# Performance work log

Measured on AMD Instinct MI355X. Metric: run time of the kernel, lower is better.

The kernel has to match this reference:

```python
import jax, jax.numpy as jnp
import numpy as np

COST_CLASS, COST_BBOX, COST_MASK = 1.0, 5.0, 2.0
EPS = 1e-6


def setup_inputs() -> dict:
    key = jax.random.key(0)
    k = jax.random.split(key, 8)
    B, Q, M, C1, H, W = 8, 300, 100, 81, 128, 128
    pred_logits = jax.random.normal(k[0], (B, Q, C1), jnp.float32)
    # boxes as valid xyxy in [0,1]: lo in [0,.5], size in [0,.5]
    plo = jax.random.uniform(k[1], (B, Q, 2)) * 0.5
    psz = jax.random.uniform(k[2], (B, Q, 2)) * 0.5
    pred_boxes = jnp.concatenate([plo, plo + psz], axis=-1)
    pred_masks = jax.random.normal(k[3], (B, Q, H, W), jnp.float32)
    gt_labels = jax.random.randint(k[4], (B, M), 0, C1, dtype=jnp.int32)
    glo = jax.random.uniform(k[5], (B, M, 2)) * 0.5
    gsz = jax.random.uniform(k[6], (B, M, 2)) * 0.5
    gt_boxes = jnp.concatenate([glo, glo + gsz], axis=-1)
    gt_masks = (jax.random.uniform(k[7], (B, M, H, W)) > 0.5).astype(jnp.float32)
    valid = jnp.ones((B, M), jnp.bool_)
    return dict(pred_logits=pred_logits, pred_boxes=pred_boxes, pred_masks=pred_masks,
                gt_labels=gt_labels, gt_boxes=gt_boxes, gt_masks=gt_masks, valid=valid)


def _giou(b1, b2):
    # b1 [Q,4], b2 [M,4] (xyxy) -> [Q,M] generalized IoU
    lt = jnp.maximum(b1[:, None, :2], b2[None, :, :2])
    rb = jnp.minimum(b1[:, None, 2:], b2[None, :, 2:])
    wh = jnp.clip(rb - lt, 0.0)
    inter = wh[..., 0] * wh[..., 1]
    a1 = (b1[:, 2] - b1[:, 0]) * (b1[:, 3] - b1[:, 1])
    a2 = (b2[:, 2] - b2[:, 0]) * (b2[:, 3] - b2[:, 1])
    union = a1[:, None] + a2[None, :] - inter
    iou = inter / (union + EPS)
    ltm = jnp.minimum(b1[:, None, :2], b2[None, :, :2])
    rbm = jnp.maximum(b1[:, None, 2:], b2[None, :, 2:])
    whm = jnp.clip(rbm - ltm, 0.0)
    am = whm[..., 0] * whm[..., 1]
    return iou - (am - union) / (am + EPS)


@jax.jit
def _cost_matrix(pred_logits, pred_boxes, pred_masks, gt_labels, gt_boxes, gt_masks):
    B, Q = pred_logits.shape[:2]
    M = gt_labels.shape[1]
    probs = jax.nn.softmax(pred_logits, axis=-1)                      # [B,Q,C+1]
    idx = jnp.broadcast_to(gt_labels[:, None, :].astype(jnp.int32), (B, Q, M))
    cost_class = -jnp.take_along_axis(probs, idx, axis=2)             # [B,Q,M]
    # L1 cdist
    cost_bbox = jnp.abs(pred_boxes[:, :, None, :] - gt_boxes[:, None, :, :]).sum(-1)
    cost_giou = -jax.vmap(_giou)(pred_boxes, gt_boxes)                # [B,Q,M]
    # dice cost
    pm = jax.nn.sigmoid(pred_masks).reshape(B, Q, -1)                 # [B,Q,HW]
    gm = gt_masks.reshape(B, M, -1).astype(pm.dtype)                  # [B,M,HW]
    num = 2.0 * jnp.einsum('bqc,bmc->bqm', pm, gm)
    den = pm.sum(-1)[:, :, None] + gm.sum(-1)[:, None, :]
    cost_mask = 1.0 - num / (den + EPS)
    # NOTE: faithful to source quirk -- giou term is folded into cost_bbox
    # and therefore weighted by COST_BBOX.
    return (COST_CLASS * cost_class + COST_BBOX * (cost_bbox + cost_giou)
            + COST_MASK * cost_mask)


def _hungarian(cost):
    # Jonker-Volgenant style shortest-augmenting-path assignment (e-maxx).
    # cost: np [n,m] with n <= m. Returns p[m]: row assigned to each col (-1 if none).
    n, m = cost.shape
    u = np.zeros(n)
    v = np.zeros(m)
    p = np.full(m, -1, np.int64)
    for i in range(n):
        minv = np.full(m, np.inf)
        way = np.full(m, -1, np.int64)
        used = np.zeros(m, bool)
        cur_row, j0 = i, -1
        while True:
            cur = cost[cur_row] - u[cur_row] - v
            upd = (~used) & (cur < minv)
            minv[upd] = cur[upd]
            way[upd] = j0
            mv = np.where(used, np.inf, minv)
            j1 = int(np.argmin(mv))
            delta = mv[j1]
            u[i] += delta
            uj = np.nonzero(used)[0]
            if uj.size:
                u[p[uj]] += delta
                v[uj] -= delta
            minv[~used] -= delta
            used[j1] = True
            j0 = j1
            cur_row = p[j1]
            if cur_row == -1:
                break
        j = j0
        while j != -1:
            jp = way[j]
            p[j] = p[jp] if jp != -1 else i
            j = jp
    return p


def reference(pred_logits, pred_boxes, pred_masks, gt_labels, gt_boxes, gt_masks, valid):
    # valid is all-ones (num_gt == max_objects for every sample), so the
    # per-sample variable-size slicing in the torch loop reduces to full M.
    C = _cost_matrix(pred_logits, pred_boxes, pred_masks, gt_labels, gt_boxes, gt_masks)
    Cn = np.asarray(C, dtype=np.float64)
    preds, gts = [], []
    for b in range(Cn.shape[0]):
        # solve on transpose: rows = gt (M=100) <= cols = queries (Q=300)
        p = _hungarian(Cn[b].T)            # p[q] = matched gt index or -1
        q = np.nonzero(p >= 0)[0]          # sorted pred indices (scipy convention)
        preds.append(q)
        gts.append(p[q])
    pred_idx = jnp.asarray(np.stack(preds), dtype=jnp.int32)  # [B, M]
    gt_idx = jnp.asarray(np.stack(gts), dtype=jnp.int32)      # [B, M]
    return C, pred_idx, gt_idx
```

## Files before the change

### kernel.cpp

```cpp
#include <hip/hip_runtime.h>

#define HW 16384
#define NQ 300
#define NM 100
#define NB 8
#define NC 81
#define KCH 4096
#define CTP 304

typedef __attribute__((ext_vector_type(8))) short frag8;
typedef __attribute__((ext_vector_type(4))) float float4v;
typedef __attribute__((ext_vector_type(4))) unsigned short ushort4v;

__device__ __forceinline__ unsigned short f2bf(float f) {
  union { float f; unsigned u; } c; c.f = f;
  unsigned r = c.u + 0x7FFFu + ((c.u >> 16) & 1u);
  return (unsigned short)(r >> 16);
}

__global__ __launch_bounds__(256) void prep_kernel(
    const float* __restrict__ pmask, const float* __restrict__ gmask,
    unsigned short* __restrict__ pm, unsigned short* __restrict__ gm,
    float* __restrict__ psum, float* __restrict__ gsum) {
  int row = blockIdx.x;
  int t = threadIdx.x;
  bool isP = row < NB * NQ;
  const float* srcf = isP ? (pmask + (size_t)row * HW)
                          : (gmask + (size_t)(row - NB * NQ) * HW);
  unsigned short* dst = isP ? (pm + (size_t)row * HW)
                            : (gm + (size_t)(row - NB * NQ) * HW);
  const float4v* src = (const float4v*)srcf;
  float s = 0.f;
  for (int i = t; i < HW / 4; i += 256) {
    float4v x = src[i];
    float y0, y1, y2, y3;
    if (isP) {
      y0 = 1.f / (1.f + __expf(-x.x));
      y1 = 1.f / (1.f + __expf(-x.y));
      y2 = 1.f / (1.f + __expf(-x.z));
      y3 = 1.f / (1.f + __expf(-x.w));
    } else { y0 = x.x; y1 = x.y; y2 = x.z; y3 = x.w; }
    s += (y0 + y1) + (y2 + y3);
    ushort4v o = { f2bf(y0), f2bf(y1), f2bf(y2), f2bf(y3) };
    *(ushort4v*)(dst + i * 4) = o;
  }
  for (int off = 32; off > 0; off >>= 1) s += __shfl_xor(s, off, 64);
  __shared__ float red[4];
  int wave = t >> 6, lane = t & 63;
  if (lane == 0) red[wave] = s;
  __syncthreads();
  if (t == 0) {
    float tot = (red[0] + red[1]) + (red[2] + red[3]);
    if (isP) psum[row] = tot; else gsum[row - NB * NQ] = tot;
  }
}

__global__ __launch_bounds__(256) void softmax_kernel(
    const float* __restrict__ logits, float* __restrict__ probs) {
  int wave = threadIdx.x >> 6, lane = threadIdx.x & 63;
  int row = blockIdx.x * 4 + wave;
  const float* in = logits + (size_t)row * NC;
  float x0 = (lane < NC) ? in[lane] : -1e30f;
  float x1 = (lane + 64 < NC) ? in[lane + 64] : -1e30f;
  float mx = fmaxf(x0, x1);
  for (int off = 32; off > 0; off >>= 1) mx = fmaxf(mx, __shfl_xor(mx, off, 64));
  float e0 = (lane < NC) ? __expf(x0 - mx) : 0.f;
  float e1 = (lane + 64 < NC) ? __expf(x1 - mx) : 0.f;
  float s = e0 + e1;
  for (int off = 32; off > 0; off >>= 1) s += __shfl_xor(s, off, 64);
  float inv = 1.f / s;
  if (lane < NC) probs[(size_t)row * NC + lane] = e0 * inv;
  if (lane + 64 < NC) probs[(size_t)row * NC + lane + 64] = e1 * inv;
}

__global__ __launch_bounds__(64) void dot_kernel(
    const unsigned short* __restrict__ pm, const unsigned short* __restrict__ gm,
    float* __restrict__ part) {
  int qt = blockIdx.x;
  int b = blockIdx.y >> 2, kc = blockIdx.y & 3;
  int lane = threadIdx.x;
  int q0 = qt * 16;
  int row_a = q0 + (lane & 15);
  int ra = (row_a < NQ) ? row_a : NQ - 1;
  int koff = (lane >> 4) * 8;
  const unsigned short* pA = pm + ((size_t)b * NQ + ra) * HW + kc * KCH + koff;
  const unsigned short* pB0 = gm + (size_t)b * NM * HW + kc * KCH + koff;
  const unsigned short* pB[7];
#pragma unroll
  for (int mt = 0; mt < 7; ++mt) {
    int row_b = mt * 16 + (lane & 15);
    int rb = (row_b < NM) ? row_b : NM - 1;
    pB[mt] = pB0 + (size_t)rb * HW;
  }
  float4v acc[7];
#pragma unroll
  for (int mt = 0; mt < 7; ++mt) acc[mt] = (float4v){0.f, 0.f, 0.f, 0.f};
#pragma unroll 2
  for (int k = 0; k < KCH; k += 32) {
    frag8 a = *(const frag8*)(pA + k);
#pragma unroll
    for (int mt = 0; mt < 7; ++mt) {
      frag8 bb = *(const frag8*)(pB[mt] + k);
      acc[mt] = __builtin_amdgcn_mfma_f32_16x16x32_bf16(a, bb, acc[mt], 0, 0, 0);
    }
  }
#pragma unroll
  for (int mt = 0; mt < 7; ++mt) {
    int cm = mt * 16 + (lane & 15);
    if (cm < NM) {
#pragma unroll
      for (int r = 0; r < 4; ++r) {
        int cq = q0 + (lane >> 4) * 4 + r;
        if (cq < NQ)
          part[(size_t)kc * (NB * NQ * NM) + ((size_t)b * NQ + cq) * NM + cm] = acc[mt][r];
      }
    }
  }
}

__global__ __launch_bounds__(256) void combine_kernel(
    const float* __restrict__ part, const float* __restrict__ psum,
    const float* __restrict__ gsum, const float* __restrict__ probs,
    const int* __restrict__ labels, const float* __restrict__ pboxes,
    const float* __restrict__ gboxes, float* __restrict__ outC,
    float* __restrict__ ct) {
  int idx = blockIdx.x * 256 + threadIdx.x;
  if (idx >= NB * NQ * NM) return;
  int b = idx / (NQ * NM);
  int r = idx - b * (NQ * NM);
  int q = r / NM;
  int m = r - q * NM;
  const int STRIDE = NB * NQ * NM;
  float num = 2.f * (part[idx] + part[STRIDE + idx] + part[2 * STRIDE + idx] + part[3 * STRIDE + idx]);
  float den = psum[b * NQ + q] + gsum[b * NM + m];
  float cmask = 1.f - num / (den + 1e-6f);
  int lab = labels[b * NM + m];
  float cclass = -probs[((size_t)b * NQ + q) * NC + lab];
  const float* pb = pboxes + ((size_t)b * NQ + q) * 4;
  const float* gb = gboxes + ((size_t)b * NM + m) * 4;
  float p0 = pb[0], p1 = pb[1], p2 = pb[2], p3 = pb[3];
  float g0 = gb[0], g1 = gb[1], g2 = gb[2], g3 = gb[3];
  float cbbox = fabsf(p0 - g0) + fabsf(p1 - g1) + fabsf(p2 - g2) + fabsf(p3 - g3);
  float iw = fmaxf(fminf(p2, g2) - fmaxf(p0, g0), 0.f);
  float ih = fmaxf(fminf(p3, g3) - fmaxf(p1, g1), 0.f);
  float inter = iw * ih;
  float a1 = (p2 - p0) * (p3 - p1), a2 = (g2 - g0) * (g3 - g1);
  float uni = a1 + a2 - inter;
  float iou = inter / (uni + 1e-6f);
  float aw = fmaxf(fmaxf(p2, g2) - fminf(p0, g0), 0.f);
  float ah = fmaxf(fmaxf(p3, g3) - fminf(p1, g1), 0.f);
  float am = aw * ah;
  float giou = iou - (am - uni) / (am + 1e-6f);
  float C = cclass + 5.f * (cbbox - giou) + 2.f * cmask;
  outC[idx] = C;
  ct[((size_t)b * NM + m) * CTP + q] = C;
}

extern __shared__ char hsmem[];
__global__ __launch_bounds__(64) void hungarian_kernel(
    const float* __restrict__ ct, float* __restrict__ out) {
  float* cost = (float*)hsmem;
  float* u = (float*)(hsmem + 121600);
  int* p = (int*)(hsmem + 122000);
  int* way = (int*)(hsmem + 123280);
  const int b = blockIdx.x;
  const int lane = threadIdx.x;
  const float* a = ct + (size_t)b * NM * CTP;

  for (int i = lane; i < NM * CTP; i += 64) cost[i] = a[i];
  for (int k = lane; k < NM; k += 64) u[k] = 0.f;
  float v[5], minv[5];
  int usedR[5];
#pragma unroll
  for (int w = 0; w < 5; ++w) {
    p[lane + 64 * w] = -1;
    v[w] = 0.f;
  }
  __syncthreads();

  for (int i = 0; i < NM; ++i) {
#pragma unroll
    for (int w = 0; w < 5; ++w) {
      int j = lane + 64 * w;
      minv[w] = __builtin_inff();
      usedR[w] = (j >= NQ) ? 1 : 0;
      way[j] = -1;
    }
    int cur_row = i;
    int j0 = -1;
    __builtin_amdgcn_wave_barrier();
    while (true) {
      float urow = u[cur_row];
      unsigned long long best = ~0ull;
#pragma unroll
      for (int w = 0; w < 5; ++w) {
        if (!usedR[w]) {
          int j = lane + 64 * w;
          float cur = cost[cur_row * CTP + j] - urow - v[w];
          if (cur < minv[w]) { minv[w] = cur; way[j] = j0; }
          unsigned sb = __float_as_uint(minv[w]);
          sb = (sb >> 31) ? ~sb : (sb | 0x80000000u);
          unsigned long long key = ((unsigned long long)sb << 32) | (unsigned)j;
          if (key < best) best = key;
        }
      }
      for (int off = 32; off > 0; off >>= 1) {
        unsigned long long o = __shfl_xor(best, off, 64);
        if (o < best) best = o;
      }
      int j1 = (int)(best & 0xFFFFFFFFu);
      unsigned sb = (unsigned)(best >> 32);
      float delta = __uint_as_float((sb >> 31) ? (sb ^ 0x80000000u) : ~sb);
      __builtin_amdgcn_wave_barrier();
#pragma unroll
      for (int w = 0; w < 5; ++w) {
        int j = lane + 64 * w;
        if (j < NQ) {
          if (usedR[w]) {
            v[w] -= delta;
            int pj = p[j];
            u[pj] += delta;
          } else {
            minv[w] -= delta;
          }
        }
      }
      if (lane == 0) u[i] += delta;
      __builtin_amdgcn_wave_barrier();
#pragma unroll
      for (int w = 0; w < 5; ++w) {
        if (lane + 64 * w == j1) usedR[w] = 1;
      }
      int nr = p[j1];
      j0 = j1;
      if (nr < 0) break;
      cur_row = nr;
    }
    __builtin_amdgcn_wave_barrier();
    if (lane == 0) {
      int j = j0;
      while (j != -1) {
        int jp = way[j];
        p[j] = (jp != -1) ? p[jp] : i;
        j = jp;
      }
    }
    __builtin_amdgcn_wave_barrier();
    __syncthreads();
  }
  if (lane == 0) {
    float* po = out + NB * NQ * NM + b * NM;
    float* go = out + NB * NQ * NM + NB * NM + b * NM;
    int cnt = 0;
    for (int j = 0; j < NQ; ++j) {
      int pj = p[j];
      if (pj >= 0) { po[cnt] = (float)j; go[cnt] = (float)pj; ++cnt; }
    }
  }
}

extern "C" void kernel_launch(void* const* d_in, const int* in_sizes, int n_in,
                              void* d_out, int out_size, void* d_ws, size_t ws_size,
                              hipStream_t stream) {
  const float* logits = (const float*)d_in[0];
  const float* pboxes = (const float*)d_in[1];
  const float* pmask  = (const float*)d_in[2];
  const int*   labels = (const int*)d_in[3];
  const float* gboxes = (const float*)d_in[4];
  const float* gmask  = (const float*)d_in[5];
  float* out = (float*)d_out;
  char* ws = (char*)d_ws;

  unsigned short* pm   = (unsigned short*)(ws + 0);
  unsigned short* gmb  = (unsigned short*)(ws + 78643200);
  float* psum  = (float*)(ws + 104857600);
  float* gsum  = (float*)(ws + 104867200);
  float* probs = (float*)(ws + 104870400);
  float* part  = (float*)(ws + 105648000);
  float* ct    = (float*)(ws + 109488000);

  static int lds_set = 0;
  (void)lds_set;
  hipFuncSetAttribute(reinterpret_cast<const void*>(hungarian_kernel),
                      hipFuncAttributeMaxDynamicSharedMemorySize, 124560);

  hipLaunchKernelGGL(prep_kernel, dim3(NB * NQ + NB * NM), dim3(256), 0, stream,
                     pmask, gmask, pm, gmb, psum, gsum);
  hipLaunchKernelGGL(softmax_kernel, dim3(600), dim3(256), 0, stream, logits, probs);
  hipLaunchKernelGGL(dot_kernel, dim3(19, NB * 4), dim3(64), 0, stream, pm, gmb, part);
  hipLaunchKernelGGL(combine_kernel, dim3((NB * NQ * NM + 255) / 256), dim3(256), 0, stream,
                     part, psum, gsum, probs, labels, pboxes, gboxes, out, ct);
  hipLaunchKernelGGL(hungarian_kernel, dim3(NB), dim3(64), 124560, stream, ct, out);
}
```

Measured before the change: 575.3 us.

## Warm-start Hungarian with greedy row minima and widen split-K with atomics

```diff
diff --git a/kernel.cpp b/kernel.cpp
--- a/kernel.cpp
+++ b/kernel.cpp
@@ -5,7 +5,8 @@
 #define NM 100
 #define NB 8
 #define NC 81
-#define KCH 4096
+#define KCH 1024
+#define NKC 16
 #define CTP 304
 
 typedef __attribute__((ext_vector_type(8))) short frag8;
@@ -75,9 +76,9 @@
 
 __global__ __launch_bounds__(64) void dot_kernel(
     const unsigned short* __restrict__ pm, const unsigned short* __restrict__ gm,
-    float* __restrict__ part) {
+    float* __restrict__ dotv) {
   int qt = blockIdx.x;
-  int b = blockIdx.y >> 2, kc = blockIdx.y & 3;
+  int b = blockIdx.y >> 4, kc = blockIdx.y & 15;
   int lane = threadIdx.x;
   int q0 = qt * 16;
   int row_a = q0 + (lane & 15);
@@ -112,14 +113,14 @@
       for (int r = 0; r < 4; ++r) {
         int cq = q0 + (lane >> 4) * 4 + r;
         if (cq < NQ)
-          part[(size_t)kc * (NB * NQ * NM) + ((size_t)b * NQ + cq) * NM + cm] = acc[mt][r];
+          unsafeAtomicAdd(&dotv[((size_t)b * NQ + cq) * NM + cm], acc[mt][r]);
       }
     }
   }
 }
 
 __global__ __launch_bounds__(256) void combine_kernel(
-    const float* __restrict__ part, const float* __restrict__ psum,
+    const float* __restrict__ dotv, const float* __restrict__ psum,
     const float* __restrict__ gsum, const float* __restrict__ probs,
     const int* __restrict__ labels, const float* __restrict__ pboxes,
     const float* __restrict__ gboxes, float* __restrict__ outC,
@@ -130,8 +131,7 @@
   int r = idx - b * (NQ * NM);
   int q = r / NM;
   int m = r - q * NM;
-  const int STRIDE = NB * NQ * NM;
-  float num = 2.f * (part[idx] + part[STRIDE + idx] + part[2 * STRIDE + idx] + part[3 * STRIDE + idx]);
+  float num = 2.f * dotv[idx];
   float den = psum[b * NQ + q] + gsum[b * NM + m];
   float cmask = 1.f - num / (den + 1e-6f);
   int lab = labels[b * NM + m];
@@ -163,22 +163,46 @@
   float* u = (float*)(hsmem + 121600);
   int* p = (int*)(hsmem + 122000);
   int* way = (int*)(hsmem + 123280);
+  int* colA = (int*)(hsmem + 124560);
+  int* rowUsed = (int*)(hsmem + 124960);
+  int* colUsed = (int*)(hsmem + 125360);
   const int b = blockIdx.x;
   const int lane = threadIdx.x;
   const float* a = ct + (size_t)b * NM * CTP;
 
   for (int i = lane; i < NM * CTP; i += 64) cost[i] = a[i];
-  for (int k = lane; k < NM; k += 64) u[k] = 0.f;
+  for (int k = lane; k < NM; k += 64) rowUsed[k] = 0;
   float v[5], minv[5];
   int usedR[5];
 #pragma unroll
   for (int w = 0; w < 5; ++w) {
     p[lane + 64 * w] = -1;
+    colUsed[lane + 64 * w] = 0;
     v[w] = 0.f;
   }
   __syncthreads();
 
+  for (int i = lane; i < NM; i += 64) {
+    float mv = __builtin_inff();
+    int cj = 0;
+    for (int j = 0; j < NQ; ++j) {
+      float c = cost[i * CTP + j];
+      if (c < mv) { mv = c; cj = j; }
+    }
+    u[i] = mv;
+    colA[i] = cj;
+  }
+  __syncthreads();
+  if (lane == 0) {
+    for (int i = 0; i < NM; ++i) {
+      int j = colA[i];
+      if (!colUsed[j]) { colUsed[j] = 1; p[j] = i; rowUsed[i] = 1; }
+    }
+  }
+  __syncthreads();
+
   for (int i = 0; i < NM; ++i) {
+    if (rowUsed[i]) continue;
 #pragma unroll
     for (int w = 0; w < 5; ++w) {
       int j = lane + 64 * w;
@@ -245,7 +269,6 @@
         j = jp;
       }
     }
-    __builtin_amdgcn_wave_barrier();
     __syncthreads();
   }
   if (lane == 0) {
@@ -276,19 +299,18 @@
   float* psum  = (float*)(ws + 104857600);
   float* gsum  = (float*)(ws + 104867200);
   float* probs = (float*)(ws + 104870400);
-  float* part  = (float*)(ws + 105648000);
-  float* ct    = (float*)(ws + 109488000);
-
-  static int lds_set = 0;
-  (void)lds_set;
+  float* dotv  = (float*)(ws + 105648000);
+  float* ct    = (float*)(ws + 106608000);
+
   hipFuncSetAttribute(reinterpret_cast<const void*>(hungarian_kernel),
-                      hipFuncAttributeMaxDynamicSharedMemorySize, 124560);
-
+                      hipFuncAttributeMaxDynamicSharedMemorySize, 126640);
+
+  hipMemsetAsync(dotv, 0, NB * NQ * NM * sizeof(float), stream);
   hipLaunchKernelGGL(prep_kernel, dim3(NB * NQ + NB * NM), dim3(256), 0, stream,
                      pmask, gmask, pm, gmb, psum, gsum);
   hipLaunchKernelGGL(softmax_kernel, dim3(600), dim3(256), 0, stream, logits, probs);
-  hipLaunchKernelGGL(dot_kernel, dim3(19, NB * 4), dim3(64), 0, stream, pm, gmb, part);
+  hipLaunchKernelGGL(dot_kernel, dim3(19, NB * NKC), dim3(64), 0, stream, pm, gmb, dotv);
   hipLaunchKernelGGL(combine_kernel, dim3((NB * NQ * NM + 255) / 256), dim3(256), 0, stream,
-                     part, psum, gsum, probs, labels, pboxes, gboxes, out, ct);
-  hipLaunchKernelGGL(hungarian_kernel, dim3(NB), dim3(64), 124560, stream, ct, out);
-}
+                     dotv, psum, gsum, probs, labels, pboxes, gboxes, out, ct);
+  hipLaunchKernelGGL(hungarian_kernel, dim3(NB), dim3(64), 126640, stream, ct, out);
+}
```

Result: faster. 516.5 us (-10.2%).
